# Performance work log

Hardware: AMD Instinct MI355X
Metric: run time of the kernel (lower is better)

## Reference

```python
import jax, jax.numpy as jnp
import numpy as np

B, F = 1024, 784
OUT, OR_T, AND_T = 1024, 32, 16
IDX_RANGE = 1 + 2 * F  # column 0 is the constant-true column


def setup_inputs() -> dict:
    key = jax.random.key(0)
    kx, kw = jax.random.split(key)
    # Binary inputs (0/1) stored as float32; module calls x.bool() i.e. x != 0.
    x = jax.random.randint(kx, (B, F), 0, 2).astype(jnp.float32)
    # Integer gate wiring: indices into [const_true | x | ~x].
    weights = jax.random.randint(kw, (OUT, OR_T, AND_T), 0, IDX_RANGE).astype(jnp.int32)
    return {"x": x, "weights": weights}


def reference(x, weights):
    out_f, or_t, and_t = weights.shape
    b = x.shape[0]
    xb = x != 0                                            # [B, F] bool
    ones = jnp.ones((b, 1), dtype=bool)
    x_in = jnp.concatenate([ones, xb, ~xb], axis=1)        # [B, 1+2F]
    # or_padding_mask: an OR-term is active unless all its AND indices are 0
    or_mask = ~jnp.all(weights == 0, axis=-1)              # [OUT, OR_T]
    # Gather selected booleans, then AND over and_terms, OR over or_terms
    x_sel = x_in[:, weights.reshape(-1)]                   # [B, OUT*OR_T*AND_T]
    x_bin = x_sel.reshape(b, out_f, or_t, and_t)
    x_and = jnp.all(x_bin, axis=-1) & or_mask              # [B, OUT, OR_T]
    x_or = jnp.any(x_and, axis=-1)                         # [B, OUT]
    return x_or
```

## Files before the change

kernel.cpp:

```cpp
#include <hip/hip_runtime.h>
#include <stdint.h>

#define BATCH 1024
#define FEAT  784
#define OUTF  1024
#define OR_T  32
#define AND_T 16
#define NIDX  1569
#define BSTRIDE 1600
#define NGROUP  16

typedef unsigned long long u64;

__global__ __launch_bounds__(64) void pack_bits(const float* __restrict__ x,
                                                u64* __restrict__ bits) {
    const int g    = blockIdx.x;
    const int fb   = blockIdx.y;
    const int lane = threadIdx.x;
    const float4* xrow = (const float4*)(x + (size_t)(g * 64 + lane) * FEAT);
    u64* bg = bits + (size_t)g * BSTRIDE;

    for (int i = 0; i < 28; ++i) {
        const int f4 = fb * 28 + i;
        const float4 v = xrow[f4];
        const int f = f4 * 4;
        const u64 m0 = __ballot(v.x != 0.0f);
        const u64 m1 = __ballot(v.y != 0.0f);
        const u64 m2 = __ballot(v.z != 0.0f);
        const u64 m3 = __ballot(v.w != 0.0f);
        if (lane == 0) {
            bg[1 + f + 0] = m0;  bg[785 + f + 0] = ~m0;
            bg[1 + f + 1] = m1;  bg[785 + f + 1] = ~m1;
            bg[1 + f + 2] = m2;  bg[785 + f + 2] = ~m2;
            bg[1 + f + 3] = m3;  bg[785 + f + 3] = ~m3;
        }
    }
    if (fb == 0 && lane == 0) bg[0] = ~0ull;
}

__global__ __launch_bounds__(256) void eval_logic(const int* __restrict__ w,
                                                  const u64* __restrict__ bits,
                                                  int* __restrict__ out) {
    __shared__ u64 lbits[BSTRIDE];
    __shared__ u64 red[256];

    const int g   = blockIdx.x;
    const int ob  = blockIdx.y;
    const int tid = threadIdx.x;

    const u64* bg = bits + (size_t)g * BSTRIDE;
    for (int i = tid; i < BSTRIDE; i += 256) lbits[i] = bg[i];
    __syncthreads();

    const int o_local = tid & 63;
    const int quad    = tid >> 6;
    const int o       = ob * 64 + o_local;

    const int4* wq = (const int4*)(w + ((size_t)o * OR_T + quad * 8) * AND_T);

    u64 orv = 0;
    for (int t = 0; t < 8; ++t) {
        u64 a = ~0ull;
        int zor = 0;
        #pragma unroll
        for (int k = 0; k < 4; ++k) {
            const int4 wi = wq[t * 4 + k];
            zor |= wi.x | wi.y | wi.z | wi.w;
            a &= lbits[wi.x];
            a &= lbits[wi.y];
            a &= lbits[wi.z];
            a &= lbits[wi.w];
        }
        if (zor != 0) orv |= a;
    }

    red[tid] = orv;
    __syncthreads();
    const u64 full = red[o_local] | red[o_local + 64] |
                     red[o_local + 128] | red[o_local + 192];

    int* outg = out + (size_t)(g * 64) * OUTF + (size_t)ob * 64;
    #pragma unroll
    for (int jj = 0; jj < 16; ++jj) {
        const int j = quad * 16 + jj;
        outg[(size_t)j * OUTF + o_local] = (int)((full >> j) & 1);
    }
}

__global__ __launch_bounds__(256) void eval_fused(const float* __restrict__ x,
                                                  const int* __restrict__ w,
                                                  int* __restrict__ out) {
    __shared__ u64 lbits[BSTRIDE];
    __shared__ u64 red[256];

    const int g   = blockIdx.x;
    const int ob  = blockIdx.y;
    const int tid = threadIdx.x;
    const int lane = tid & 63;
    const int wv   = tid >> 6;

    const float4* xrow = (const float4*)(x + (size_t)(g * 64 + lane) * FEAT);
    for (int i = 0; i < 49; ++i) {
        const int f4 = wv * 49 + i;
        const float4 v = xrow[f4];
        const int f = f4 * 4;
        const u64 m0 = __ballot(v.x != 0.0f);
        const u64 m1 = __ballot(v.y != 0.0f);
        const u64 m2 = __ballot(v.z != 0.0f);
        const u64 m3 = __ballot(v.w != 0.0f);
        if (lane == 0) {
            lbits[1 + f + 0] = m0;  lbits[785 + f + 0] = ~m0;
            lbits[1 + f + 1] = m1;  lbits[785 + f + 1] = ~m1;
            lbits[1 + f + 2] = m2;  lbits[785 + f + 2] = ~m2;
            lbits[1 + f + 3] = m3;  lbits[785 + f + 3] = ~m3;
        }
    }
    if (tid == 0) lbits[0] = ~0ull;
    __syncthreads();

    const int o_local = tid & 63;
    const int quad    = tid >> 6;
    const int o       = ob * 64 + o_local;
    const int4* wq = (const int4*)(w + ((size_t)o * OR_T + quad * 8) * AND_T);

    u64 orv = 0;
    for (int t = 0; t < 8; ++t) {
        u64 a = ~0ull;
        int zor = 0;
        #pragma unroll
        for (int k = 0; k < 4; ++k) {
            const int4 wi = wq[t * 4 + k];
            zor |= wi.x | wi.y | wi.z | wi.w;
            a &= lbits[wi.x];
            a &= lbits[wi.y];
            a &= lbits[wi.z];
            a &= lbits[wi.w];
        }
        if (zor != 0) orv |= a;
    }

    red[tid] = orv;
    __syncthreads();
    const u64 full = red[o_local] | red[o_local + 64] |
                     red[o_local + 128] | red[o_local + 192];

    int* outg = out + (size_t)(g * 64) * OUTF + (size_t)ob * 64;
    #pragma unroll
    for (int jj = 0; jj < 16; ++jj) {
        const int j = quad * 16 + jj;
        outg[(size_t)j * OUTF + o_local] = (int)((full >> j) & 1);
    }
}

extern "C" void kernel_launch(void* const* d_in, const int* in_sizes, int n_in,
                              void* d_out, int out_size, void* d_ws, size_t ws_size,
                              hipStream_t stream) {
    const float* x = (const float*)d_in[0];
    const int*   w = (const int*)d_in[1];
    int* out = (int*)d_out;

    const size_t need = (size_t)NGROUP * BSTRIDE * sizeof(u64);
    if (ws_size >= need) {
        u64* bits = (u64*)d_ws;
        pack_bits<<<dim3(NGROUP, 7), 64, 0, stream>>>(x, bits);
        eval_logic<<<dim3(NGROUP, OUTF / 64), 256, 0, stream>>>(w, bits, out);
    } else {
        eval_fused<<<dim3(NGROUP, OUTF / 64), 256, 0, stream>>>(x, w, out);
    }
}
```

Baseline: 74.22 us.

## Fuse bit packing into one 1024-thread kernel splitting OR terms across waves

Replaces the two-kernel path (pack bits to workspace, then evaluate) with a single fused kernel using 1024 threads per block. Sixteen waves jointly pack the 64-row bit slab into shared memory, and each wave evaluates two OR terms per output, followed by a 16-way shared-memory OR reduction. This removes a launch and the global round-trip for packed bits, and raises parallelism per block. In exchange every block redundantly packs its x slab (16x across output blocks), and the large blocks may limit occupancy.

```diff
diff --git a/kernel.cpp b/kernel.cpp
--- a/kernel.cpp
+++ b/kernel.cpp
@@ -7,64 +7,56 @@
 #define OR_T  32
 #define AND_T 16
 #define NIDX  1569
-#define BSTRIDE 1600
-#define NGROUP  16
+#define LWORDS 1600
 
 typedef unsigned long long u64;
 
-__global__ __launch_bounds__(64) void pack_bits(const float* __restrict__ x,
-                                                u64* __restrict__ bits) {
+__global__ __launch_bounds__(1024) void binlayer(const float* __restrict__ x,
+                                                 const int* __restrict__ w,
+                                                 int* __restrict__ out) {
+    __shared__ u64 lbits[LWORDS];
+    __shared__ u64 red[1024];
+
     const int g    = blockIdx.x;
-    const int fb   = blockIdx.y;
-    const int lane = threadIdx.x;
+    const int ob   = blockIdx.y;
+    const int tid  = threadIdx.x;
+    const int lane = tid & 63;
+    const int wv   = tid >> 6;
+
+    const int start = wv * 12 + (wv < 4 ? wv : 4);
+    const int cnt   = (wv < 4) ? 13 : 12;
     const float4* xrow = (const float4*)(x + (size_t)(g * 64 + lane) * FEAT);
-    u64* bg = bits + (size_t)g * BSTRIDE;
-
-    for (int i = 0; i < 28; ++i) {
-        const int f4 = fb * 28 + i;
+    for (int i = 0; i < cnt; ++i) {
+        const int f4 = start + i;
         const float4 v = xrow[f4];
         const int f = f4 * 4;
         const u64 m0 = __ballot(v.x != 0.0f);
         const u64 m1 = __ballot(v.y != 0.0f);
         const u64 m2 = __ballot(v.z != 0.0f);
         const u64 m3 = __ballot(v.w != 0.0f);
-        if (lane == 0) {
-            bg[1 + f + 0] = m0;  bg[785 + f + 0] = ~m0;
-            bg[1 + f + 1] = m1;  bg[785 + f + 1] = ~m1;
-            bg[1 + f + 2] = m2;  bg[785 + f + 2] = ~m2;
-            bg[1 + f + 3] = m3;  bg[785 + f + 3] = ~m3;
+        const u64 mv = (lane == 0) ? m0 : (lane == 1) ? m1 : (lane == 2) ? m2 : m3;
+        if (lane < 4) {
+            lbits[1 + f + lane]   = mv;
+            lbits[785 + f + lane] = ~mv;
         }
     }
-    if (fb == 0 && lane == 0) bg[0] = ~0ull;
-}
-
-__global__ __launch_bounds__(256) void eval_logic(const int* __restrict__ w,
-                                                  const u64* __restrict__ bits,
-                                                  int* __restrict__ out) {
-    __shared__ u64 lbits[BSTRIDE];
-    __shared__ u64 red[256];
-
-    const int g   = blockIdx.x;
-    const int ob  = blockIdx.y;
-    const int tid = threadIdx.x;
-
-    const u64* bg = bits + (size_t)g * BSTRIDE;
-    for (int i = tid; i < BSTRIDE; i += 256) lbits[i] = bg[i];
+    if (tid == 0) lbits[0] = ~0ull;
     __syncthreads();
 
     const int o_local = tid & 63;
-    const int quad    = tid >> 6;
+    const int tg      = tid >> 6;
     const int o       = ob * 64 + o_local;
 
-    const int4* wq = (const int4*)(w + ((size_t)o * OR_T + quad * 8) * AND_T);
+    const int4* wq = (const int4*)(w + ((size_t)o * OR_T + tg * 2) * AND_T);
 
     u64 orv = 0;
-    for (int t = 0; t < 8; ++t) {
+    #pragma unroll
+    for (int tt = 0; tt < 2; ++tt) {
         u64 a = ~0ull;
         int zor = 0;
         #pragma unroll
         for (int k = 0; k < 4; ++k) {
-            const int4 wi = wq[t * 4 + k];
+            const int4 wi = wq[tt * 4 + k];
             zor |= wi.x | wi.y | wi.z | wi.w;
             a &= lbits[wi.x];
             a &= lbits[wi.y];
@@ -76,78 +68,15 @@
 
     red[tid] = orv;
     __syncthreads();
-    const u64 full = red[o_local] | red[o_local + 64] |
-                     red[o_local + 128] | red[o_local + 192];
+
+    u64 full = 0;
+    #pragma unroll
+    for (int j = 0; j < 16; ++j) full |= red[o_local + j * 64];
 
     int* outg = out + (size_t)(g * 64) * OUTF + (size_t)ob * 64;
     #pragma unroll
-    for (int jj = 0; jj < 16; ++jj) {
-        const int j = quad * 16 + jj;
-        outg[(size_t)j * OUTF + o_local] = (int)((full >> j) & 1);
-    }
-}
-
-__global__ __launch_bounds__(256) void eval_fused(const float* __restrict__ x,
-                                                  const int* __restrict__ w,
-                                                  int* __restrict__ out) {
-    __shared__ u64 lbits[BSTRIDE];
-    __shared__ u64 red[256];
-
-    const int g   = blockIdx.x;
-    const int ob  = blockIdx.y;
-    const int tid = threadIdx.x;
-    const int lane = tid & 63;
-    const int wv   = tid >> 6;
-
-    const float4* xrow = (const float4*)(x + (size_t)(g * 64 + lane) * FEAT);
-    for (int i = 0; i < 49; ++i) {
-        const int f4 = wv * 49 + i;
-        const float4 v = xrow[f4];
-        const int f = f4 * 4;
-        const u64 m0 = __ballot(v.x != 0.0f);
-        const u64 m1 = __ballot(v.y != 0.0f);
-        const u64 m2 = __ballot(v.z != 0.0f);
-        const u64 m3 = __ballot(v.w != 0.0f);
-        if (lane == 0) {
-            lbits[1 + f + 0] = m0;  lbits[785 + f + 0] = ~m0;
-            lbits[1 + f + 1] = m1;  lbits[785 + f + 1] = ~m1;
-            lbits[1 + f + 2] = m2;  lbits[785 + f + 2] = ~m2;
-            lbits[1 + f + 3] = m3;  lbits[785 + f + 3] = ~m3;
-        }
-    }
-    if (tid == 0) lbits[0] = ~0ull;
-    __syncthreads();
-
-    const int o_local = tid & 63;
-    const int quad    = tid >> 6;
-    const int o       = ob * 64 + o_local;
-    const int4* wq = (const int4*)(w + ((size_t)o * OR_T + quad * 8) * AND_T);
-
-    u64 orv = 0;
-    for (int t = 0; t < 8; ++t) {
-        u64 a = ~0ull;
-        int zor = 0;
-        #pragma unroll
-        for (int k = 0; k < 4; ++k) {
-            const int4 wi = wq[t * 4 + k];
-            zor |= wi.x | wi.y | wi.z | wi.w;
-            a &= lbits[wi.x];
-            a &= lbits[wi.y];
-            a &= lbits[wi.z];
-            a &= lbits[wi.w];
-        }
-        if (zor != 0) orv |= a;
-    }
-
-    red[tid] = orv;
-    __syncthreads();
-    const u64 full = red[o_local] | red[o_local + 64] |
-                     red[o_local + 128] | red[o_local + 192];
-
-    int* outg = out + (size_t)(g * 64) * OUTF + (size_t)ob * 64;
-    #pragma unroll
-    for (int jj = 0; jj < 16; ++jj) {
-        const int j = quad * 16 + jj;
+    for (int jj = 0; jj < 4; ++jj) {
+        const int j = tg * 4 + jj;
         outg[(size_t)j * OUTF + o_local] = (int)((full >> j) & 1);
     }
 }
@@ -159,12 +88,5 @@
     const int*   w = (const int*)d_in[1];
     int* out = (int*)d_out;
 
-    const size_t need = (size_t)NGROUP * BSTRIDE * sizeof(u64);
-    if (ws_size >= need) {
-        u64* bits = (u64*)d_ws;
-        pack_bits<<<dim3(NGROUP, 7), 64, 0, stream>>>(x, bits);
-        eval_logic<<<dim3(NGROUP, OUTF / 64), 256, 0, stream>>>(w, bits, out);
-    } else {
-        eval_fused<<<dim3(NGROUP, OUTF / 64), 256, 0, stream>>>(x, w, out);
-    }
+    binlayer<<<dim3(BATCH / 64, OUTF / 64), 1024, 0, stream>>>(x, w, out);
 }
```

After: 75.34 us. Within noise of the previous version (+1.5%).
